# Kernel optimization log

Measured on AMD Instinct MI355X. Metric: run time of the kernel, lower is better.

## Reference

```python
import jax, jax.numpy as jnp
import numpy as np

TOP_K = 8
ROUTED_SCALING_FACTOR = 1.0
EPS = 1e-20


def setup_inputs() -> dict:
    key = jax.random.key(0)
    k1, k2, k3 = jax.random.split(key, 3)
    T, D, E = 8192, 4096, 64
    x = jax.random.normal(k1, (T, D), dtype=jnp.float32)
    gate_weight = jax.random.normal(k2, (E, D), dtype=jnp.float32) * (1.0 / np.sqrt(D))
    bias = jax.random.normal(k3, (E,), dtype=jnp.float32) * 0.1
    return {"x": x, "gate_weight": gate_weight, "bias": bias}


def reference(x, gate_weight, bias):
    # logits: [T, E] = x [T, D] @ gate_weight.T [D, E]
    logits = jnp.einsum('td,ed->te', x.astype(jnp.float32), gate_weight)
    scores = jax.nn.sigmoid(logits)
    biased = scores + bias  # broadcast [E]
    # top-k on biased scores, sorted descending
    _, indices = jax.lax.top_k(biased, TOP_K)  # [T, K]
    selected_scores = jnp.take_along_axis(scores, indices, axis=-1)  # [T, K]
    normalized = selected_scores / (jnp.sum(selected_scores, axis=-1, keepdims=True) + EPS)
    weights = normalized * ROUTED_SCALING_FACTOR
    return (indices, weights)
```

## Files before the change

### kernel.cpp

```cpp
#include <hip/hip_runtime.h>
#include <math.h>
#include <stdint.h>

#define T_TOK 8192
#define DDIM  4096
#define NEXP  64
#define TOPK  8
#define MT    128
#define BK    32
#define RS    2048.0f

typedef __attribute__((ext_vector_type(8))) _Float16 half8;
typedef __attribute__((ext_vector_type(4))) float f32x4;
typedef __attribute__((address_space(3))) uint32_t lds_u32;
typedef const __attribute__((address_space(1))) uint32_t glb_u32;

__global__ __launch_bounds__(256) void pack_w(
    const float* __restrict__ gw, _Float16* __restrict__ wpk)
{
    const int g    = blockIdx.x * 256 + threadIdx.x;
    const int lane = g & 63;
    const int n    = (g >> 6) & 3;
    const int kt   = g >> 8;
    const int e    = n * 16 + (lane & 15);
    const int k    = kt * 32 + (lane >> 4) * 8;

    const float* src = gw + (size_t)e * DDIM + k;
    float4 v0 = *reinterpret_cast<const float4*>(src);
    float4 v1 = *reinterpret_cast<const float4*>(src + 4);
    const float v[8] = {v0.x, v0.y, v0.z, v0.w, v1.x, v1.y, v1.z, v1.w};

    half8 h0, h1;
    #pragma unroll
    for (int j = 0; j < 8; j++) {
        _Float16 a = (_Float16)v[j];
        h0[j] = a;
        h1[j] = (_Float16)((v[j] - (float)a) * RS);
    }
    _Float16* dst = wpk + (size_t)kt * 4096 + (size_t)(n * 2) * 512 + lane * 8;
    *reinterpret_cast<half8*>(dst)       = h0;
    *reinterpret_cast<half8*>(dst + 512) = h1;
}

template<int STEPS>
__global__ __launch_bounds__(512, 4) void gemm_part(
    const float* __restrict__ x, const _Float16* __restrict__ wpk,
    float* __restrict__ part)
{
    __shared__ float    A[3][MT * BK];
    __shared__ _Float16 B[3][4096];

    const int tid  = threadIdx.x;
    const int lane = tid & 63;
    const int wv   = tid >> 6;
    const int wm   = wv & 3;
    const int wn   = wv >> 2;
    const int mt   = blockIdx.x & 63;
    const int slc  = blockIdx.x >> 6;
    const int m0   = mt * MT;
    const int kt0  = slc * STEPS;
    const int am   = lane & 15;
    const int ag   = lane >> 4;

    const int s_row0 = tid >> 3;
    const int s_c    = tid & 7;

#define STAGE(buf_, t_) do {                                                   \
        const size_t koff = (size_t)(kt0 + (t_)) * BK;                         \
        int c0 = s_c ^ (s_row0 & 7);                                           \
        __builtin_amdgcn_global_load_lds(                                      \
            (glb_u32*)(x + (size_t)(m0 + s_row0) * DDIM + koff + c0 * 4),      \
            (lds_u32*)(&A[buf_][tid * 4]), 16, 0, 0);                          \
        int r1 = s_row0 + 64;                                                  \
        int c1 = s_c ^ (r1 & 7);                                               \
        __builtin_amdgcn_global_load_lds(                                      \
            (glb_u32*)(x + (size_t)(m0 + r1) * DDIM + koff + c1 * 4),          \
            (lds_u32*)(&A[buf_][2048 + tid * 4]), 16, 0, 0);                   \
        const _Float16* bs = wpk + (size_t)(kt0 + (t_)) * 4096 + tid * 8;      \
        __builtin_amdgcn_global_load_lds(                                      \
            (glb_u32*)bs, (lds_u32*)(&B[buf_][tid * 8]), 16, 0, 0);            \
    } while (0)

    f32x4 aH[2][2], aM[2][2];
    #pragma unroll
    for (int f = 0; f < 2; f++)
        #pragma unroll
        for (int n = 0; n < 2; n++) {
            aH[f][n] = (f32x4){0.f, 0.f, 0.f, 0.f};
            aM[f][n] = (f32x4){0.f, 0.f, 0.f, 0.f};
        }

    auto compute = [&](int buf) {
        half8 B0[2], B1[2];
        #pragma unroll
        for (int nf = 0; nf < 2; nf++) {
            const int nb = ((wn * 2 + nf) * 2) * 512 + lane * 8;
            B0[nf] = *reinterpret_cast<const half8*>(&B[buf][nb]);
            B1[nf] = *reinterpret_cast<const half8*>(&B[buf][nb + 512]);
        }
        #pragma unroll
        for (int f = 0; f < 2; f++) {
            const int row = wm * 32 + f * 16 + am;
            const int sw  = am & 7;
            float4 alo = *reinterpret_cast<const float4*>(
                &A[buf][row * BK + ((ag * 2 + 0) ^ sw) * 4]);
            float4 ahi = *reinterpret_cast<const float4*>(
                &A[buf][row * BK + ((ag * 2 + 1) ^ sw) * 4]);
            const float vv[8] = {alo.x, alo.y, alo.z, alo.w,
                                 ahi.x, ahi.y, ahi.z, ahi.w};
            half8 a0, a1;
            #pragma unroll
            for (int j = 0; j < 8; j++) {
                float v = vv[j];
                _Float16 h = (_Float16)v;
                a0[j] = h;
                a1[j] = (_Float16)((v - (float)h) * RS);
            }
            #pragma unroll
            for (int nf = 0; nf < 2; nf++) {
                aH[f][nf] = __builtin_amdgcn_mfma_f32_16x16x32_f16(a0, B0[nf], aH[f][nf], 0, 0, 0);
                aM[f][nf] = __builtin_amdgcn_mfma_f32_16x16x32_f16(a0, B1[nf], aM[f][nf], 0, 0, 0);
                aM[f][nf] = __builtin_amdgcn_mfma_f32_16x16x32_f16(a1, B0[nf], aM[f][nf], 0, 0, 0);
            }
        }
    };

    STAGE(0, 0);
    STAGE(1, 1);

    for (int t = 0; t < STEPS - 1; t++) {
        asm volatile("s_waitcnt vmcnt(3)" ::: "memory");
        __builtin_amdgcn_sched_barrier(0);
        __builtin_amdgcn_s_barrier();
        __builtin_amdgcn_sched_barrier(0);
        if (t + 2 < STEPS) STAGE((t + 2) % 3, t + 2);
        compute(t % 3);
    }
    asm volatile("s_waitcnt vmcnt(0)" ::: "memory");
    __builtin_amdgcn_sched_barrier(0);
    __builtin_amdgcn_s_barrier();
    __builtin_amdgcn_sched_barrier(0);
    compute((STEPS - 1) % 3);
#undef STAGE

    const float i1 = 1.0f / RS;
    float* po = part + (size_t)slc * T_TOK * NEXP + (size_t)m0 * NEXP;
    #pragma unroll
    for (int f = 0; f < 2; f++)
        #pragma unroll
        for (int nf = 0; nf < 2; nf++)
            #pragma unroll
            for (int r = 0; r < 4; r++)
                po[(size_t)(wm * 32 + f * 16 + ag * 4 + r) * NEXP
                   + (wn * 2 + nf) * 16 + am]
                    = aH[f][nf][r] + aM[f][nf][r] * i1;
}

__global__ __launch_bounds__(256) void reduce_topk(
    const float* __restrict__ part, const float* __restrict__ bias,
    float* __restrict__ out, int S)
{
    const int wave = threadIdx.x >> 6;
    const int lane = threadIdx.x & 63;
    const int j    = blockIdx.x;
    const int g    = j & 7;
    const int q    = j >> 3;
    const int token = g * 128 + (q & 31) * 4 + (q >> 5) * 1024 + wave;
    if (token >= T_TOK) return;

    float logit = 0.f;
    for (int s = 0; s < S; s++)
        logit += part[(size_t)s * T_TOK * NEXP + (size_t)token * NEXP + lane];

    float score  = 1.f / (1.f + expf(-logit));
    float biased = score + bias[lane];

    float my_sc = 0.f;
    int   my_idx = 0;
    float ssum  = 0.f;

    #pragma unroll
    for (int jj = 0; jj < TOPK; jj++) {
        float v = biased;
        int   i = lane;
        #pragma unroll
        for (int off = 32; off >= 1; off >>= 1) {
            float ov = __shfl_xor(v, off);
            int   oi = __shfl_xor(i, off);
            if (ov > v || (ov == v && oi < i)) { v = ov; i = oi; }
        }
        float s_sel = __shfl(score, i);
        ssum += s_sel;
        if (lane == jj) { my_idx = i; my_sc = s_sel; }
        if (lane == i) biased = -INFINITY;
    }

    if (lane < TOPK) {
        out[(size_t)token * TOPK + lane] = (float)my_idx;
        out[(size_t)T_TOK * TOPK + (size_t)token * TOPK + lane]
            = my_sc / (ssum + 1e-20f);
    }
}

extern "C" void kernel_launch(void* const* d_in, const int* in_sizes, int n_in,
                              void* d_out, int out_size, void* d_ws, size_t ws_size,
                              hipStream_t stream) {
    (void)in_sizes; (void)n_in; (void)out_size;
    const float* x    = (const float*)d_in[0];
    const float* gw   = (const float*)d_in[1];
    const float* bias = (const float*)d_in[2];
    float* out = (float*)d_out;
    _Float16* wpk = (_Float16*)d_ws;
    float* part = (float*)(wpk + (size_t)DDIM * NEXP * 2);

    const size_t wpk_bytes = (size_t)DDIM * NEXP * 2 * sizeof(_Float16);
    const size_t per_slice = (size_t)T_TOK * NEXP * sizeof(float);
    int S = 1;
    for (int cand : {8, 4, 2}) {
        if (wpk_bytes + (size_t)cand * per_slice <= ws_size) { S = cand; break; }
    }

    pack_w<<<128, 256, 0, stream>>>(gw, wpk);

    dim3 b1(512);
    switch (S) {
        case 8: gemm_part<16><<<dim3(64 * 8), b1, 0, stream>>>(x, wpk, part); break;
        case 4: gemm_part<32><<<dim3(64 * 4), b1, 0, stream>>>(x, wpk, part); break;
        case 2: gemm_part<64><<<dim3(64 * 2), b1, 0, stream>>>(x, wpk, part); break;
        default: gemm_part<128><<<dim3(64), b1, 0, stream>>>(x, wpk, part); break;
    }

    reduce_topk<<<dim3(T_TOK / 4), 256, 0, stream>>>(part, bias, out, S);
}
```

Measured before the change: 48.98 us.

## Switch GEMM to double-buffered syncthreads pipeline and interleave K-slices per tile

Replaces the triple-buffered LDS pipeline, which used explicit vmcnt waits and raw barriers, with a simpler double-buffered loop that issues the next stage before computing and ends each step with __syncthreads. Block indexing now puts the K-slices of one M tile in consecutive blocks so they run at the same time, and the min-blocks launch bound is dropped. The intent is lower LDS use and possibly better cache locality, but the full barrier each step and the single prefetch stage give less room to hide load latency.

```diff
diff --git a/kernel.cpp b/kernel.cpp
--- a/kernel.cpp
+++ b/kernel.cpp
@@ -42,21 +42,21 @@
     *reinterpret_cast<half8*>(dst + 512) = h1;
 }
 
-template<int STEPS>
-__global__ __launch_bounds__(512, 4) void gemm_part(
+template<int STEPS, int S>
+__global__ __launch_bounds__(512) void gemm_part(
     const float* __restrict__ x, const _Float16* __restrict__ wpk,
     float* __restrict__ part)
 {
-    __shared__ float    A[3][MT * BK];
-    __shared__ _Float16 B[3][4096];
+    __shared__ float    A[2][MT * BK];
+    __shared__ _Float16 B[2][4096];
 
     const int tid  = threadIdx.x;
     const int lane = tid & 63;
     const int wv   = tid >> 6;
     const int wm   = wv & 3;
     const int wn   = wv >> 2;
-    const int mt   = blockIdx.x & 63;
-    const int slc  = blockIdx.x >> 6;
+    const int slc  = blockIdx.x % S;
+    const int mt   = blockIdx.x / S;
     const int m0   = mt * MT;
     const int kt0  = slc * STEPS;
     const int am   = lane & 15;
@@ -90,7 +90,14 @@
             aM[f][n] = (f32x4){0.f, 0.f, 0.f, 0.f};
         }
 
-    auto compute = [&](int buf) {
+    STAGE(0, 0);
+    __syncthreads();
+
+    #pragma unroll 2
+    for (int t = 0; t < STEPS; t++) {
+        const int buf = t & 1;
+        if (t + 1 < STEPS) STAGE(buf ^ 1, t + 1);
+
         half8 B0[2], B1[2];
         #pragma unroll
         for (int nf = 0; nf < 2; nf++) {
@@ -123,24 +130,8 @@
                 aM[f][nf] = __builtin_amdgcn_mfma_f32_16x16x32_f16(a1, B0[nf], aM[f][nf], 0, 0, 0);
             }
         }
-    };
-
-    STAGE(0, 0);
-    STAGE(1, 1);
-
-    for (int t = 0; t < STEPS - 1; t++) {
-        asm volatile("s_waitcnt vmcnt(3)" ::: "memory");
-        __builtin_amdgcn_sched_barrier(0);
-        __builtin_amdgcn_s_barrier();
-        __builtin_amdgcn_sched_barrier(0);
-        if (t + 2 < STEPS) STAGE((t + 2) % 3, t + 2);
-        compute(t % 3);
-    }
-    asm volatile("s_waitcnt vmcnt(0)" ::: "memory");
-    __builtin_amdgcn_sched_barrier(0);
-    __builtin_amdgcn_s_barrier();
-    __builtin_amdgcn_sched_barrier(0);
-    compute((STEPS - 1) % 3);
+        __syncthreads();
+    }
 #undef STAGE
 
     const float i1 = 1.0f / RS;
@@ -224,10 +215,10 @@
 
     dim3 b1(512);
     switch (S) {
-        case 8: gemm_part<16><<<dim3(64 * 8), b1, 0, stream>>>(x, wpk, part); break;
-        case 4: gemm_part<32><<<dim3(64 * 4), b1, 0, stream>>>(x, wpk, part); break;
-        case 2: gemm_part<64><<<dim3(64 * 2), b1, 0, stream>>>(x, wpk, part); break;
-        default: gemm_part<128><<<dim3(64), b1, 0, stream>>>(x, wpk, part); break;
+        case 8: gemm_part<16, 8><<<dim3(64 * 8), b1, 0, stream>>>(x, wpk, part); break;
+        case 4: gemm_part<32, 4><<<dim3(64 * 4), b1, 0, stream>>>(x, wpk, part); break;
+        case 2: gemm_part<64, 2><<<dim3(64 * 2), b1, 0, stream>>>(x, wpk, part); break;
+        default: gemm_part<128, 1><<<dim3(64), b1, 0, stream>>>(x, wpk, part); break;
     }
 
     reduce_topk<<<dim3(T_TOK / 4), 256, 0, stream>>>(part, bias, out, S);
```

Result: faster. 47.28 us (-3.5%).
